# Kernel optimization log

Measured on AMD Instinct MI355X. Metric: run time of the kernel, lower is better.

## Reference

```python
import jax, jax.numpy as jnp
import numpy as np
import math

B, T, D = 2, 2048, 4096
H, HD = 32, 128  # n_head, head_dim; H*HD == D
THETA = 10000.0


def _rope_tables(T, hd, theta):
    # standard RoPE: freqs_i = theta^(-2i/hd), angle[t,i] = t * freqs_i
    inv = 1.0 / (theta ** (np.arange(0, hd, 2, dtype=np.float32) / hd))  # [hd/2]
    ang = np.arange(T, dtype=np.float32)[:, None] * inv[None, :]          # [T, hd/2]
    return jnp.asarray(np.cos(ang)), jnp.asarray(np.sin(ang))


def setup_inputs() -> dict:
    key = jax.random.key(0)
    ks = jax.random.split(key, 5)
    scale = 1.0 / math.sqrt(D)
    x = jax.random.normal(ks[0], (B, T, D), dtype=jnp.float32)
    Wq = jax.random.normal(ks[1], (D, H * HD), dtype=jnp.float32) * scale
    Wk = jax.random.normal(ks[2], (D, H * HD), dtype=jnp.float32) * scale
    Wv = jax.random.normal(ks[3], (D, H * HD), dtype=jnp.float32) * scale
    Wo = jax.random.normal(ks[4], (D, D), dtype=jnp.float32) * scale
    fc, fs = _rope_tables(T, HD, THETA)
    return {"x": x, "freqs_cos": fc, "freqs_sin": fs,
            "Wq": Wq, "Wk": Wk, "Wv": Wv, "Wo": Wo}


def _apply_rope(t, cos, sin):
    # t: [B, T, H, HD]; complex rotation on interleaved (even, odd) pairs
    tp = t.reshape(*t.shape[:-1], HD // 2, 2)
    xr, xi = tp[..., 0], tp[..., 1]
    c = cos[None, :, None, :]  # [1, T, 1, HD/2]
    s = sin[None, :, None, :]
    out_r = xr * c - xi * s
    out_i = xr * s + xi * c
    return jnp.stack([out_r, out_i], axis=-1).reshape(t.shape)


def reference(x, freqs_cos, freqs_sin, Wq, Wk, Wv, Wo):
    Bc, Tc, _ = x.shape
    q = (x @ Wq).reshape(Bc, Tc, H, HD)
    k = (x @ Wk).reshape(Bc, Tc, H, HD)
    v = (x @ Wv).reshape(Bc, Tc, H, HD)
    q = _apply_rope(q, freqs_cos, freqs_sin)
    k = _apply_rope(k, freqs_cos, freqs_sin)
    scale = 1.0 / math.sqrt(HD)
    scores = jnp.einsum('bqhd,bkhd->bhqk', q, k) * scale  # [B,H,T,T]
    causal = jnp.tril(jnp.ones((Tc, Tc), dtype=bool))
    scores = jnp.where(causal[None, None], scores, -jnp.inf)
    attn = jax.nn.softmax(scores, axis=-1)
    y = jnp.einsum('bhqk,bkhd->bqhd', attn, v).reshape(Bc, Tc, H * HD)
    return y @ Wo
```

## Files before the change

### kernel.cpp

```cpp
#include <hip/hip_runtime.h>

typedef unsigned short ushort_t;
typedef unsigned int uint32;

typedef float f32x4 __attribute__((ext_vector_type(4)));
typedef __bf16 bf16x8 __attribute__((ext_vector_type(8)));
typedef unsigned short us8 __attribute__((ext_vector_type(8)));
typedef unsigned short us4 __attribute__((ext_vector_type(4)));

#define TSEQ 2048
#define DMODEL 4096

__device__ __forceinline__ ushort_t f2bf(float f) {
  uint32 u = __builtin_bit_cast(uint32, f);
  u += 0x7FFFu + ((u >> 16) & 1u);
  return (ushort_t)(u >> 16);
}
__device__ __forceinline__ float bf2f(ushort_t u) {
  return __builtin_bit_cast(float, ((uint32)u) << 16);
}

__device__ __forceinline__ void gload_lds16(const void* g, void* l) {
  auto gp = (const __attribute__((address_space(1))) void*)g;
  auto lp = (__attribute__((address_space(3))) void*)l;
  __builtin_amdgcn_global_load_lds(gp, lp, 16, 0, 0);
}

__global__ __launch_bounds__(256) void k_cast_bf16(const float* __restrict__ in,
                                                   ushort_t* __restrict__ out, int n4) {
  int g = blockIdx.x * 256 + threadIdx.x;
  if (g >= n4) return;
  float4 v = *(const float4*)(in + (size_t)g * 4);
  us4 o; o[0] = f2bf(v.x); o[1] = f2bf(v.y); o[2] = f2bf(v.z); o[3] = f2bf(v.w);
  *(us4*)(out + (size_t)g * 4) = o;
}

__global__ __launch_bounds__(256) void k_transpose_cast(const float* __restrict__ W,
                                                        ushort_t* __restrict__ WT) {
  __shared__ __align__(16) ushort_t ts[64 * 72];
  const int tid = threadIdx.x;
  const int n0 = blockIdx.x * 64, k0 = blockIdx.y * 64;
  #pragma unroll
  for (int it = 0; it < 4; ++it) {
    int e = it * 256 + tid;
    int r = e >> 4, c4 = e & 15;
    float4 v = *(const float4*)(W + (size_t)(k0 + r) * DMODEL + n0 + c4 * 4);
    us4 o; o[0] = f2bf(v.x); o[1] = f2bf(v.y); o[2] = f2bf(v.z); o[3] = f2bf(v.w);
    *(us4*)&ts[r * 72 + c4 * 4] = o;
  }
  __syncthreads();
  #pragma unroll
  for (int it = 0; it < 4; ++it) {
    int e = it * 256 + tid;
    int r2 = e >> 4, c4 = e & 15;
    us4 o;
    #pragma unroll
    for (int j = 0; j < 4; ++j) o[j] = ts[(c4 * 4 + j) * 72 + r2];
    *(us4*)(WT + (size_t)(n0 + r2) * DMODEL + k0 + c4 * 4) = o;
  }
}

template <bool OUT_BF16>
__global__ __launch_bounds__(512, 2)
void k_gemm256(const ushort_t* __restrict__ A, const ushort_t* __restrict__ Bt,
               void* __restrict__ Cv, int M, int N, int K) {
  __shared__ __align__(16) ushort_t As[2][256 * 64];
  __shared__ __align__(16) ushort_t Bs[2][256 * 64];
  const int tid = threadIdx.x;
  const int w = tid >> 6, l = tid & 63;
  const int wr = w >> 2, wc = w & 3;
  const int lg = l >> 4, lc = l & 15;

  const int nwg = gridDim.x;
  const int cpx = nwg >> 3;
  const int wg = (blockIdx.x & 7) * cpx + (blockIdx.x >> 3);
  const int nbn = N >> 8;
  const int bm = wg / nbn, bn = wg % nbn;

  const int rowoff = l >> 3;
  const int swzck  = (l & 7) ^ rowoff;
  const ushort_t* Ab = A + (size_t)(bm * 256) * K;
  const ushort_t* Bb = Bt + (size_t)(bn * 256) * K;
  const ushort_t* gA[4]; const ushort_t* gB[4];
  int ldsOff[4];
  #pragma unroll
  for (int j = 0; j < 4; ++j) {
    int r0 = (w * 4 + j) * 8;
    gA[j] = Ab + (size_t)(r0 + rowoff) * K + swzck * 8;
    gB[j] = Bb + (size_t)(r0 + rowoff) * K + swzck * 8;
    ldsOff[j] = r0 * 64;
  }

  int offA[8][2], offB[4][2];
  #pragma unroll
  for (int m = 0; m < 8; ++m)
    #pragma unroll
    for (int kk = 0; kk < 2; ++kk)
      offA[m][kk] = (wr * 128 + m * 16 + lc) * 64 + (((kk * 4 + lg) ^ (lc & 7)) * 8);
  #pragma unroll
  for (int n = 0; n < 4; ++n)
    #pragma unroll
    for (int kk = 0; kk < 2; ++kk)
      offB[n][kk] = (wc * 64 + n * 16 + lc) * 64 + (((kk * 4 + lg) ^ (lc & 7)) * 8);

  f32x4 acc[8][4];
  #pragma unroll
  for (int m = 0; m < 8; ++m)
    #pragma unroll
    for (int n = 0; n < 4; ++n) acc[m][n] = (f32x4){0.f, 0.f, 0.f, 0.f};

  #pragma unroll
  for (int j = 0; j < 4; ++j) {
    gload_lds16(gA[j], &As[0][ldsOff[j]]);
    gload_lds16(gB[j], &Bs[0][ldsOff[j]]);
  }
  #pragma unroll
  for (int j = 0; j < 4; ++j) {
    gload_lds16(gA[j] + 64, &As[1][ldsOff[j]]);
    gload_lds16(gB[j] + 64, &Bs[1][ldsOff[j]]);
  }
  asm volatile("s_waitcnt vmcnt(8)" ::: "memory");
  __builtin_amdgcn_s_barrier();
  __builtin_amdgcn_sched_barrier(0);

  const int NT = K >> 6;
  for (int t = 0; t < NT; ++t) {
    const int cur = t & 1;
    const ushort_t* Ac = As[cur];
    const ushort_t* Bc = Bs[cur];
    bf16x8 af[4][2], bf0[2][2], bf1[2][2];

    #pragma unroll
    for (int i = 0; i < 4; ++i)
      #pragma unroll
      for (int kk = 0; kk < 2; ++kk)
        af[i][kk] = *(const bf16x8*)&Ac[offA[i][kk]];
    #pragma unroll
    for (int j2 = 0; j2 < 2; ++j2)
      #pragma unroll
      for (int kk = 0; kk < 2; ++kk)
        bf0[j2][kk] = *(const bf16x8*)&Bc[offB[j2][kk]];
    asm volatile("" ::: "memory");
    __builtin_amdgcn_s_barrier();
    __builtin_amdgcn_s_setprio(1);
    #pragma unroll
    for (int i = 0; i < 4; ++i)
      #pragma unroll
      for (int j2 = 0; j2 < 2; ++j2)
        #pragma unroll
        for (int kk = 0; kk < 2; ++kk)
          acc[i][j2] = __builtin_amdgcn_mfma_f32_16x16x32_bf16(af[i][kk], bf0[j2][kk], acc[i][j2], 0, 0, 0);
    __builtin_amdgcn_s_setprio(0);
    __builtin_amdgcn_s_barrier();
    asm volatile("" ::: "memory");

    #pragma unroll
    for (int j2 = 0; j2 < 2; ++j2)
      #pragma unroll
      for (int kk = 0; kk < 2; ++kk)
        bf1[j2][kk] = *(const bf16x8*)&Bc[offB[2 + j2][kk]];
    asm volatile("" ::: "memory");
    __builtin_amdgcn_s_barrier();
    __builtin_amdgcn_s_setprio(1);
    #pragma unroll
    for (int i = 0; i < 4; ++i)
      #pragma unroll
      for (int j2 = 0; j2 < 2; ++j2)
        #pragma unroll
        for (int kk = 0; kk < 2; ++kk)
          acc[i][2 + j2] = __builtin_amdgcn_mfma_f32_16x16x32_bf16(af[i][kk], bf1[j2][kk], acc[i][2 + j2], 0, 0, 0);
    __builtin_amdgcn_s_setprio(0);
    __builtin_amdgcn_s_barrier();
    asm volatile("" ::: "memory");

    #pragma unroll
    for (int i = 0; i < 4; ++i)
      #pragma unroll
      for (int kk = 0; kk < 2; ++kk)
        af[i][kk] = *(const bf16x8*)&Ac[offA[4 + i][kk]];
    asm volatile("" ::: "memory");
    __builtin_amdgcn_s_barrier();
    __builtin_amdgcn_s_setprio(1);
    #pragma unroll
    for (int i = 0; i < 4; ++i)
      #pragma unroll
      for (int j2 = 0; j2 < 2; ++j2)
        #pragma unroll
        for (int kk = 0; kk < 2; ++kk)
          acc[4 + i][j2] = __builtin_amdgcn_mfma_f32_16x16x32_bf16(af[i][kk], bf0[j2][kk], acc[4 + i][j2], 0, 0, 0);
    __builtin_amdgcn_s_setprio(0);
    __builtin_amdgcn_s_barrier();
    asm volatile("" ::: "memory");

    if (t + 2 < NT) {
      const int k0 = (t + 2) << 6;
      #pragma unroll
      for (int j = 0; j < 4; ++j) {
        gload_lds16(gA[j] + k0, &As[cur][ldsOff[j]]);
        gload_lds16(gB[j] + k0, &Bs[cur][ldsOff[j]]);
      }
    }
    asm volatile("" ::: "memory");
    __builtin_amdgcn_s_barrier();
    __builtin_amdgcn_s_setprio(1);
    #pragma unroll
    for (int i = 0; i < 4; ++i)
      #pragma unroll
      for (int j2 = 0; j2 < 2; ++j2)
        #pragma unroll
        for (int kk = 0; kk < 2; ++kk)
          acc[4 + i][2 + j2] = __builtin_amdgcn_mfma_f32_16x16x32_bf16(af[i][kk], bf1[j2][kk], acc[4 + i][2 + j2], 0, 0, 0);
    __builtin_amdgcn_s_setprio(0);

    if (t + 2 < NT) {
      asm volatile("s_waitcnt vmcnt(8)" ::: "memory");
    } else if (t + 1 < NT) {
      asm volatile("s_waitcnt vmcnt(0)" ::: "memory");
    }
    if (t + 1 < NT) {
      __builtin_amdgcn_s_barrier();
      __builtin_amdgcn_sched_barrier(0);
    }
  }

  #pragma unroll
  for (int m = 0; m < 8; ++m) {
    int row0 = bm * 256 + wr * 128 + m * 16 + lg * 4;
    #pragma unroll
    for (int n = 0; n < 4; ++n) {
      int col = bn * 256 + wc * 64 + n * 16 + lc;
      #pragma unroll
      for (int r = 0; r < 4; ++r) {
        float v = acc[m][n][r];
        if (OUT_BF16) ((ushort_t*)Cv)[(size_t)(row0 + r) * N + col] = f2bf(v);
        else          ((float*)Cv)[(size_t)(row0 + r) * N + col] = v;
      }
    }
  }
}

__global__ __launch_bounds__(256) void k_rope(ushort_t* __restrict__ q, ushort_t* __restrict__ k,
                                              const float* __restrict__ fc,
                                              const float* __restrict__ fs) {
  int g = blockIdx.x * 256 + threadIdx.x;
  size_t base = (size_t)g * 8;
  int row = (int)(base >> 12);
  int col = (int)(base & 4095);
  int t = row & (TSEQ - 1);
  int i0 = (col & 127) >> 1;
  float4 c = *(const float4*)(fc + t * 64 + i0);
  float4 s = *(const float4*)(fs + t * 64 + i0);
  ushort_t* bufs[2] = {q, k};
  #pragma unroll
  for (int bi = 0; bi < 2; ++bi) {
    us8 v = *(const us8*)(bufs[bi] + base);
    us8 o;
    float xr, xi;
    xr = bf2f(v[0]); xi = bf2f(v[1]);
    o[0] = f2bf(xr * c.x - xi * s.x); o[1] = f2bf(xr * s.x + xi * c.x);
    xr = bf2f(v[2]); xi = bf2f(v[3]);
    o[2] = f2bf(xr * c.y - xi * s.y); o[3] = f2bf(xr * s.y + xi * c.y);
    xr = bf2f(v[4]); xi = bf2f(v[5]);
    o[4] = f2bf(xr * c.z - xi * s.z); o[5] = f2bf(xr * s.z + xi * c.z);
    xr = bf2f(v[6]); xi = bf2f(v[7]);
    o[6] = f2bf(xr * c.w - xi * s.w); o[7] = f2bf(xr * s.w + xi * c.w);
    *(us8*)(bufs[bi] + base) = o;
  }
}

__global__ __launch_bounds__(256, 2)
void k_attn(const ushort_t* __restrict__ Q, const ushort_t* __restrict__ Kb,
            const ushort_t* __restrict__ Vt, ushort_t* __restrict__ Y) {
  __shared__ __align__(16) ushort_t Ks[64 * 128];
  __shared__ __align__(16) ushort_t Vs[128 * 64];
  __shared__ __align__(16) ushort_t Ps[4][16 * 64];
  const int bx = blockIdx.x, h = blockIdx.y, b = blockIdx.z;
  const int tid = threadIdx.x;
  const int w = tid >> 6, l = tid & 63;
  const int lg = l >> 4, lc = l & 15;
  const float scale = 0.08838834764831845f;

  for (int qi = 0; qi < 2; ++qi) {
    const int qt = qi ? (31 - bx) : bx;
    const int q0 = qt * 64;

    bf16x8 qf[4];
    {
      const ushort_t* qp = Q + (size_t)(b * TSEQ + q0 + w * 16 + lc) * DMODEL + h * 128;
      #pragma unroll
      for (int ks = 0; ks < 4; ++ks) qf[ks] = *(const bf16x8*)(qp + ks * 32 + lg * 8);
    }

    float m_r[4], l_r[4];
    #pragma unroll
    for (int r = 0; r < 4; ++r) { m_r[r] = -1e30f; l_r[r] = 0.f; }
    f32x4 o[8];
    #pragma unroll
    for (int t = 0; t < 8; ++t) o[t] = (f32x4){0.f, 0.f, 0.f, 0.f};

    for (int kt = 0; kt <= qt; ++kt) {
      const int kv0 = kt * 64;
      #pragma unroll
      for (int i = 0; i < 4; ++i) {
        int cdx = tid + i * 256;
        int row = cdx >> 4, ch = cdx & 15;
        us8 v = *(const us8*)(Kb + (size_t)(b * TSEQ + kv0 + row) * DMODEL + h * 128 + ch * 8);
        *(us8*)&Ks[row * 128 + ((ch * 8) ^ ((row & 7) * 8))] = v;
      }
      #pragma unroll
      for (int i = 0; i < 4; ++i) {
        int cdx = tid + i * 256;
        int row = cdx >> 3, ch = cdx & 7;
        us8 v = *(const us8*)(Vt + (size_t)(h * 128 + row) * DMODEL + b * TSEQ + kv0 + ch * 8);
        *(us8*)&Vs[row * 64 + ((ch * 8) ^ ((row & 7) * 8))] = v;
      }
      __syncthreads();

      f32x4 s[4];
      __builtin_amdgcn_s_setprio(1);
      #pragma unroll
      for (int n = 0; n < 4; ++n) {
        s[n] = (f32x4){0.f, 0.f, 0.f, 0.f};
        #pragma unroll
        for (int ks = 0; ks < 4; ++ks) {
          int row = n * 16 + lc;
          bf16x8 kf = *(const bf16x8*)&Ks[row * 128 + ((ks * 32 + lg * 8) ^ ((row & 7) * 8))];
          s[n] = __builtin_amdgcn_mfma_f32_16x16x32_bf16(qf[ks], kf, s[n], 0, 0, 0);
        }
      }
      __builtin_amdgcn_s_setprio(0);

      const bool diag = (kt == qt);
      float pv[4][4];
      #pragma unroll
      for (int r = 0; r < 4; ++r) {
        float mx = -1e30f;
        #pragma unroll
        for (int n = 0; n < 4; ++n) {
          float sv = s[n][r] * scale;
          if (diag) {
            int kvg = n * 16 + lc;
            int qg = w * 16 + lg * 4 + r;
            if (kvg > qg) sv = -1e30f;
          }
          pv[n][r] = sv;
          mx = fmaxf(mx, sv);
        }
        #pragma unroll
        for (int off = 1; off < 16; off <<= 1) mx = fmaxf(mx, __shfl_xor(mx, off, 16));
        float mn = fmaxf(m_r[r], mx);
        float al = __expf(m_r[r] - mn);
        m_r[r] = mn;
        float ls = 0.f;
        #pragma unroll
        for (int n = 0; n < 4; ++n) { float p = __expf(pv[n][r] - mn); pv[n][r] = p; ls += p; }
        #pragma unroll
        for (int off = 1; off < 16; off <<= 1) ls += __shfl_xor(ls, off, 16);
        l_r[r] = l_r[r] * al + ls;
        #pragma unroll
        for (int t = 0; t < 8; ++t) o[t][r] *= al;
      }

      #pragma unroll
      for (int n = 0; n < 4; ++n)
        #pragma unroll
        for (int r = 0; r < 4; ++r) {
          int row = lg * 4 + r, col = n * 16 + lc;
          Ps[w][row * 64 + (col ^ ((row & 7) * 8))] = f2bf(pv[n][r]);
        }

      __builtin_amdgcn_s_setprio(1);
      #pragma unroll
      for (int kvs = 0; kvs < 2; ++kvs) {
        bf16x8 pa = *(const bf16x8*)&Ps[w][lc * 64 + ((kvs * 32 + lg * 8) ^ ((lc & 7) * 8))];
        #pragma unroll
        for (int t = 0; t < 8; ++t) {
          int vrow = t * 16 + lc;
          bf16x8 vb = *(const bf16x8*)&Vs[vrow * 64 + ((kvs * 32 + lg * 8) ^ ((vrow & 7) * 8))];
          o[t] = __builtin_amdgcn_mfma_f32_16x16x32_bf16(pa, vb, o[t], 0, 0, 0);
        }
      }
      __builtin_amdgcn_s_setprio(0);
      __syncthreads();
    }

    #pragma unroll
    for (int t = 0; t < 8; ++t)
      #pragma unroll
      for (int r = 0; r < 4; ++r) {
        int row = q0 + w * 16 + lg * 4 + r;
        int col = h * 128 + t * 16 + lc;
        Y[(size_t)(b * TSEQ + row) * DMODEL + col] = f2bf(o[t][r] / l_r[r]);
      }
  }
}

extern "C" void kernel_launch(void* const* d_in, const int* in_sizes, int n_in,
                              void* d_out, int out_size, void* d_ws, size_t ws_size,
                              hipStream_t stream) {
  const float* x  = (const float*)d_in[0];
  const float* fc = (const float*)d_in[1];
  const float* fs = (const float*)d_in[2];
  const float* Wq = (const float*)d_in[3];
  const float* Wk = (const float*)d_in[4];
  const float* Wv = (const float*)d_in[5];
  const float* Wo = (const float*)d_in[6];

  const size_t SZ = (size_t)4096 * 4096;
  ushort_t* xb  = (ushort_t*)d_ws;
  ushort_t* WqT = xb + SZ;
  ushort_t* WkT = WqT + SZ;
  ushort_t* WvT = WkT + SZ;
  ushort_t* WoT = WvT + SZ;
  ushort_t* qb  = WoT + SZ;
  ushort_t* kb  = qb + SZ;
  ushort_t* vT  = kb + SZ;
  ushort_t* yb  = vT + SZ;

  k_cast_bf16<<<16384, 256, 0, stream>>>(x, xb, 4194304);
  dim3 tg(64, 64);
  k_transpose_cast<<<tg, 256, 0, stream>>>(Wq, WqT);
  k_transpose_cast<<<tg, 256, 0, stream>>>(Wk, WkT);
  k_transpose_cast<<<tg, 256, 0, stream>>>(Wv, WvT);
  k_transpose_cast<<<tg, 256, 0, stream>>>(Wo, WoT);

  k_gemm256<true><<<256, 512, 0, stream>>>(xb, WqT, qb, 4096, 4096, 4096);
  k_gemm256<true><<<256, 512, 0, stream>>>(xb, WkT, kb, 4096, 4096, 4096);
  k_gemm256<true><<<256, 512, 0, stream>>>(WvT, xb, vT, 4096, 4096, 4096);

  k_rope<<<8192, 256, 0, stream>>>(qb, kb, fc, fs);

  dim3 ag(16, 32, 2);
  k_attn<<<ag, 256, 0, stream>>>(qb, kb, vT, yb);

  k_gemm256<false><<<256, 512, 0, stream>>>(yb, WoT, d_out, 4096, 4096, 4096);
}
```

Baseline: 939.3 us.

## Widen attention query tile to 128 rows, add lazy softmax rescaling

The attention kernel now uses 512-thread blocks that cover 128 query rows per tile, so each K/V tile loaded into shared memory is reused by twice as many warps. Warps whose rows lie entirely before a KV tile skip its compute. Online softmax now rescales only when some row's new max exceeds the running max by more than a threshold, and the row-sum reduction is deferred to the end. This cuts exp/shuffle work per tile, at the cost of more idle warps on diagonal tiles and fewer blocks in the grid.

Result: no change. 954.4 us (+1.6%).

```diff
diff --git a/kernel.cpp b/kernel.cpp
--- a/kernel.cpp
+++ b/kernel.cpp
@@ -268,129 +268,153 @@
   }
 }
 
-__global__ __launch_bounds__(256, 2)
+__global__ __launch_bounds__(512, 2)
 void k_attn(const ushort_t* __restrict__ Q, const ushort_t* __restrict__ Kb,
             const ushort_t* __restrict__ Vt, ushort_t* __restrict__ Y) {
   __shared__ __align__(16) ushort_t Ks[64 * 128];
   __shared__ __align__(16) ushort_t Vs[128 * 64];
-  __shared__ __align__(16) ushort_t Ps[4][16 * 64];
+  __shared__ __align__(16) ushort_t Ps[8][16 * 64];
   const int bx = blockIdx.x, h = blockIdx.y, b = blockIdx.z;
   const int tid = threadIdx.x;
   const int w = tid >> 6, l = tid & 63;
   const int lg = l >> 4, lc = l & 15;
   const float scale = 0.08838834764831845f;
+  const float THR = 8.0f;
 
   for (int qi = 0; qi < 2; ++qi) {
-    const int qt = qi ? (31 - bx) : bx;
-    const int q0 = qt * 64;
+    const int qt = qi ? (15 - bx) : bx;
+    const int q0 = qt * 128;
+    const int wrow0 = q0 + w * 16;
 
     bf16x8 qf[4];
     {
-      const ushort_t* qp = Q + (size_t)(b * TSEQ + q0 + w * 16 + lc) * DMODEL + h * 128;
+      const ushort_t* qp = Q + (size_t)(b * TSEQ + wrow0 + lc) * DMODEL + h * 128;
       #pragma unroll
       for (int ks = 0; ks < 4; ++ks) qf[ks] = *(const bf16x8*)(qp + ks * 32 + lg * 8);
     }
 
-    float m_r[4], l_r[4];
-    #pragma unroll
-    for (int r = 0; r < 4; ++r) { m_r[r] = -1e30f; l_r[r] = 0.f; }
+    float m_r[4], lp[4];
+    #pragma unroll
+    for (int r = 0; r < 4; ++r) { m_r[r] = -1e30f; lp[r] = 0.f; }
     f32x4 o[8];
     #pragma unroll
     for (int t = 0; t < 8; ++t) o[t] = (f32x4){0.f, 0.f, 0.f, 0.f};
 
-    for (int kt = 0; kt <= qt; ++kt) {
+    const int nkv = (qt + 1) * 2;
+    for (int kt = 0; kt < nkv; ++kt) {
       const int kv0 = kt * 64;
       #pragma unroll
-      for (int i = 0; i < 4; ++i) {
-        int cdx = tid + i * 256;
+      for (int i = 0; i < 2; ++i) {
+        int cdx = tid + i * 512;
         int row = cdx >> 4, ch = cdx & 15;
         us8 v = *(const us8*)(Kb + (size_t)(b * TSEQ + kv0 + row) * DMODEL + h * 128 + ch * 8);
         *(us8*)&Ks[row * 128 + ((ch * 8) ^ ((row & 7) * 8))] = v;
       }
       #pragma unroll
-      for (int i = 0; i < 4; ++i) {
-        int cdx = tid + i * 256;
+      for (int i = 0; i < 2; ++i) {
+        int cdx = tid + i * 512;
         int row = cdx >> 3, ch = cdx & 7;
         us8 v = *(const us8*)(Vt + (size_t)(h * 128 + row) * DMODEL + b * TSEQ + kv0 + ch * 8);
         *(us8*)&Vs[row * 64 + ((ch * 8) ^ ((row & 7) * 8))] = v;
       }
       __syncthreads();
 
-      f32x4 s[4];
-      __builtin_amdgcn_s_setprio(1);
-      #pragma unroll
-      for (int n = 0; n < 4; ++n) {
-        s[n] = (f32x4){0.f, 0.f, 0.f, 0.f};
-        #pragma unroll
-        for (int ks = 0; ks < 4; ++ks) {
-          int row = n * 16 + lc;
-          bf16x8 kf = *(const bf16x8*)&Ks[row * 128 + ((ks * 32 + lg * 8) ^ ((row & 7) * 8))];
-          s[n] = __builtin_amdgcn_mfma_f32_16x16x32_bf16(qf[ks], kf, s[n], 0, 0, 0);
+      if (kv0 <= wrow0 + 15) {
+        f32x4 s[4];
+        __builtin_amdgcn_s_setprio(1);
+        #pragma unroll
+        for (int n = 0; n < 4; ++n) {
+          s[n] = (f32x4){0.f, 0.f, 0.f, 0.f};
+          #pragma unroll
+          for (int ks = 0; ks < 4; ++ks) {
+            int row = n * 16 + lc;
+            bf16x8 kf = *(const bf16x8*)&Ks[row * 128 + ((ks * 32 + lg * 8) ^ ((row & 7) * 8))];
+            s[n] = __builtin_amdgcn_mfma_f32_16x16x32_bf16(qf[ks], kf, s[n], 0, 0, 0);
+          }
         }
-      }
-      __builtin_amdgcn_s_setprio(0);
-
-      const bool diag = (kt == qt);
-      float pv[4][4];
+        __builtin_amdgcn_s_setprio(0);
+
+        float sv[4][4];
+        if (kv0 + 63 > wrow0) {
+          #pragma unroll
+          for (int n = 0; n < 4; ++n)
+            #pragma unroll
+            for (int r = 0; r < 4; ++r) {
+              float x = s[n][r] * scale;
+              int kvg = kv0 + n * 16 + lc;
+              int qg = wrow0 + lg * 4 + r;
+              sv[n][r] = (kvg > qg) ? -1e30f : x;
+            }
+        } else {
+          #pragma unroll
+          for (int n = 0; n < 4; ++n)
+            #pragma unroll
+            for (int r = 0; r < 4; ++r) sv[n][r] = s[n][r] * scale;
+        }
+
+        float pmax[4];
+        #pragma unroll
+        for (int r = 0; r < 4; ++r)
+          pmax[r] = fmaxf(fmaxf(sv[0][r], sv[1][r]), fmaxf(sv[2][r], sv[3][r]));
+        bool ok = (pmax[0] <= m_r[0] + THR) && (pmax[1] <= m_r[1] + THR) &&
+                  (pmax[2] <= m_r[2] + THR) && (pmax[3] <= m_r[3] + THR);
+        if (!__all(ok)) {
+          #pragma unroll
+          for (int r = 0; r < 4; ++r) {
+            float mx = pmax[r];
+            #pragma unroll
+            for (int off = 1; off < 16; off <<= 1) mx = fmaxf(mx, __shfl_xor(mx, off, 16));
+            float mn = fmaxf(m_r[r], mx);
+            float al = __expf(m_r[r] - mn);
+            m_r[r] = mn;
+            lp[r] *= al;
+            #pragma unroll
+            for (int t = 0; t < 8; ++t) o[t][r] *= al;
+          }
+        }
+
+        #pragma unroll
+        for (int n = 0; n < 4; ++n)
+          #pragma unroll
+          for (int r = 0; r < 4; ++r) {
+            float p = __expf(sv[n][r] - m_r[r]);
+            lp[r] += p;
+            int row = lg * 4 + r, col = n * 16 + lc;
+            Ps[w][row * 64 + (col ^ ((row & 7) * 8))] = f2bf(p);
+          }
+
+        __builtin_amdgcn_s_setprio(1);
+        #pragma unroll
+        for (int kvs = 0; kvs < 2; ++kvs) {
+          bf16x8 pa = *(const bf16x8*)&Ps[w][lc * 64 + ((kvs * 32 + lg * 8) ^ ((lc & 7) * 8))];
+          #pragma unroll
+          for (int t = 0; t < 8; ++t) {
+            int vrow = t * 16 + lc;
+            bf16x8 vb = *(const bf16x8*)&Vs[vrow * 64 + ((kvs * 32 + lg * 8) ^ ((vrow & 7) * 8))];
+            o[t] = __builtin_amdgcn_mfma_f32_16x16x32_bf16(pa, vb, o[t], 0, 0, 0);
+          }
+        }
+        __builtin_amdgcn_s_setprio(0);
+      }
+      __syncthreads();
+    }
+
+    float linv[4];
+    #pragma unroll
+    for (int r = 0; r < 4; ++r) {
+      float ls = lp[r];
+      #pragma unroll
+      for (int off = 1; off < 16; off <<= 1) ls += __shfl_xor(ls, off, 16);
+      linv[r] = 1.0f / ls;
+    }
+
+    #pragma unroll
+    for (int t = 0; t < 8; ++t)
       #pragma unroll
       for (int r = 0; r < 4; ++r) {
-        float mx = -1e30f;
-        #pragma unroll
-        for (int n = 0; n < 4; ++n) {
-          float sv = s[n][r] * scale;
-          if (diag) {
-            int kvg = n * 16 + lc;
-            int qg = w * 16 + lg * 4 + r;
-            if (kvg > qg) sv = -1e30f;
-          }
-          pv[n][r] = sv;
-          mx = fmaxf(mx, sv);
-        }
-        #pragma unroll
-        for (int off = 1; off < 16; off <<= 1) mx = fmaxf(mx, __shfl_xor(mx, off, 16));
-        float mn = fmaxf(m_r[r], mx);
-        float al = __expf(m_r[r] - mn);
-        m_r[r] = mn;
-        float ls = 0.f;
-        #pragma unroll
-        for (int n = 0; n < 4; ++n) { float p = __expf(pv[n][r] - mn); pv[n][r] = p; ls += p; }
-        #pragma unroll
-        for (int off = 1; off < 16; off <<= 1) ls += __shfl_xor(ls, off, 16);
-        l_r[r] = l_r[r] * al + ls;
-        #pragma unroll
-        for (int t = 0; t < 8; ++t) o[t][r] *= al;
-      }
-
-      #pragma unroll
-      for (int n = 0; n < 4; ++n)
-        #pragma unroll
-        for (int r = 0; r < 4; ++r) {
-          int row = lg * 4 + r, col = n * 16 + lc;
-          Ps[w][row * 64 + (col ^ ((row & 7) * 8))] = f2bf(pv[n][r]);
-        }
-
-      __builtin_amdgcn_s_setprio(1);
-      #pragma unroll
-      for (int kvs = 0; kvs < 2; ++kvs) {
-        bf16x8 pa = *(const bf16x8*)&Ps[w][lc * 64 + ((kvs * 32 + lg * 8) ^ ((lc & 7) * 8))];
-        #pragma unroll
-        for (int t = 0; t < 8; ++t) {
-          int vrow = t * 16 + lc;
-          bf16x8 vb = *(const bf16x8*)&Vs[vrow * 64 + ((kvs * 32 + lg * 8) ^ ((vrow & 7) * 8))];
-          o[t] = __builtin_amdgcn_mfma_f32_16x16x32_bf16(pa, vb, o[t], 0, 0, 0);
-        }
-      }
-      __builtin_amdgcn_s_setprio(0);
-      __syncthreads();
-    }
-
-    #pragma unroll
-    for (int t = 0; t < 8; ++t)
-      #pragma unroll
-      for (int r = 0; r < 4; ++r) {
-        int row = q0 + w * 16 + lg * 4 + r;
+        int row = wrow0 + lg * 4 + r;
         int col = h * 128 + t * 16 + lc;
-        Y[(size_t)(b * TSEQ + row) * DMODEL + col] = f2bf(o[t][r] / l_r[r]);
+        Y[(size_t)(b * TSEQ + row) * DMODEL + col] = f2bf(o[t][r] * linv[r]);
       }
   }
 }
@@ -430,8 +454,8 @@
 
   k_rope<<<8192, 256, 0, stream>>>(qb, kb, fc, fs);
 
-  dim3 ag(16, 32, 2);
-  k_attn<<<ag, 256, 0, stream>>>(qb, kb, vT, yb);
+  dim3 ag(8, 32, 2);
+  k_attn<<<ag, 512, 0, stream>>>(qb, kb, vT, yb);
 
   k_gemm256<false><<<256, 512, 0, stream>>>(yb, WoT, d_out, 4096, 4096, 4096);
 }
```
